# Optimization experiments

Measured on AMD Instinct MI355X. Metric: run time of the kernel, lower is better.

The kernel has to match this reference:

```python
import jax, jax.numpy as jnp
import numpy as np

INPUT_DIM = 6
HIDDEN = 128


def neighbor_mean(x, adj):
    # x: [B,N,F], adj: [B,N,N]; node i averages itself + neighbors (adj>0)
    mask = (adj > 0).astype(x.dtype)  # [B,N,N]
    s = jnp.einsum('bij,bjf->bif', mask, x) + x  # sum neighbors + self
    cnt = mask.sum(-1) + 1.0  # [B,N]
    return s / cnt[..., None]


def lstm_scan(x, Wi, Wh, bi, bh, reverse=False):
    # x: [B,T,F]; Wi: [4H,F]; Wh: [4H,H]; gate order i,f,g,o (torch)
    B, T, F = x.shape
    H = Wh.shape[1]
    xw = jnp.einsum('btf,gf->btg', x, Wi) + bi + bh  # [B,T,4H]
    def step(carry, xt):
        h, c = carry
        z = xt + h @ Wh.T  # [B,4H]
        i, f, g, o = jnp.split(z, 4, axis=-1)
        i = jax.nn.sigmoid(i); f = jax.nn.sigmoid(f)
        g = jnp.tanh(g); o = jax.nn.sigmoid(o)
        c = f * c + i * g
        h = o * jnp.tanh(c)
        return (h, c), h
    init = (jnp.zeros((B, H), x.dtype), jnp.zeros((B, H), x.dtype))
    xs = jnp.swapaxes(xw, 0, 1)  # [T,B,4H]
    (hT, cT), hs = jax.lax.scan(step, init, xs, reverse=reverse)
    return hT


def setup_inputs():
    key = jax.random.key(0)
    ks = jax.random.split(key, 12)
    B, N = 4096, 64
    inp = {
        'device_idx': jax.random.uniform(ks[0], (B,), jnp.float32),
        'matrix': jax.random.uniform(ks[1], (B, N, N), jnp.float32),
        'features': jax.random.normal(ks[2], (B, N, INPUT_DIM), jnp.float32),
    }
    s = 1.0 / np.sqrt(HIDDEN)
    def u(k, shape):
        return jax.random.uniform(k, shape, jnp.float32, -s, s)
    inp['Wi_f'] = u(ks[3], (4 * HIDDEN, INPUT_DIM))
    inp['Wh_f'] = u(ks[4], (4 * HIDDEN, HIDDEN))
    inp['bi_f'] = u(ks[5], (4 * HIDDEN,))
    inp['bh_f'] = u(ks[6], (4 * HIDDEN,))
    inp['Wi_b'] = u(ks[7], (4 * HIDDEN, INPUT_DIM))
    inp['Wh_b'] = u(ks[8], (4 * HIDDEN, HIDDEN))
    inp['bi_b'] = u(ks[9], (4 * HIDDEN,))
    inp['bh_b'] = u(ks[10], (4 * HIDDEN,))
    inp['fc_w'] = u(ks[11], (1, 2 * HIDDEN + 1))
    inp['fc_b'] = jnp.zeros((1,), jnp.float32)
    return inp


def reference(device_idx, matrix, features, Wi_f, Wh_f, bi_f, bh_f, Wi_b, Wh_b, bi_b, bh_b, fc_w, fc_b):
    upd = neighbor_mean(features, matrix)  # [B,N,6]
    h_fwd = lstm_scan(upd, Wi_f, Wh_f, bi_f, bh_f, reverse=False)  # [B,H]
    h_bwd = lstm_scan(upd, Wi_b, Wh_b, bi_b, bh_b, reverse=True)   # [B,H]
    hn = jnp.concatenate([h_fwd, h_bwd], axis=1)  # [B,2H]
    final = jnp.concatenate([device_idx[:, None], hn], axis=1)  # [B,2H+1]
    y = final @ fc_w.T + fc_b
    return y.reshape(-1)
```

## Files before the change

kernel.cpp:

```cpp
#include <hip/hip_runtime.h>
#include <hip/hip_bf16.h>

#define B_TOTAL 4096

typedef short short8 __attribute__((ext_vector_type(8)));
typedef float f32x4 __attribute__((ext_vector_type(4)));
typedef int   i32x4 __attribute__((ext_vector_type(4)));

__device__ __forceinline__ unsigned short rne_bf16(float x) {
    unsigned int u = __float_as_uint(x);
    unsigned int r = (u + 0x7fffu + ((u >> 16) & 1u)) >> 16;
    return (unsigned short)r;
}
__device__ __forceinline__ unsigned int cvt2bf(float lo, float hi) {
    unsigned int r;
    asm("v_cvt_pk_bf16_f32 %0, %1, %2" : "=v"(r) : "v"(lo), "v"(hi));
    return r;
}
__device__ __forceinline__ float fast_sigm(float x) {
    return __builtin_amdgcn_rcpf(1.0f + __expf(-x));
}
__device__ __forceinline__ float fast_tanh(float x) {
    return 1.0f - 2.0f * __builtin_amdgcn_rcpf(1.0f + __expf(2.0f * x));
}
__device__ __forceinline__ void cell_update(const f32x4 z, float& c, float& h) {
    const float ig = fast_sigm(z[0]);
    const float fg = fast_sigm(z[1]);
    const float gg = fast_tanh(z[2]);
    const float og = fast_sigm(z[3]);
    c = fg * c + ig * gg;
    h = og * fast_tanh(c);
}

__global__ __launch_bounds__(256) void k_neighbor_mean(
    const float* __restrict__ matrix,
    const float* __restrict__ features,
    float* __restrict__ upd)
{
    __shared__ float adj[64][65];
    __shared__ float fx[64][6];
    const int b = blockIdx.x;
    const int tid = threadIdx.x;
    const float* mb_ = matrix + (size_t)b * 4096;
    for (int idx = tid; idx < 4096; idx += 256) adj[idx >> 6][idx & 63] = mb_[idx];
    const float* fb = features + (size_t)b * 384;
    for (int idx = tid; idx < 384; idx += 256) fx[idx / 6][idx % 6] = fb[idx];
    __syncthreads();
    if (tid < 64) {
        const int i = tid;
        float s0=0,s1=0,s2=0,s3=0,s4=0,s5=0,cnt=0;
        for (int j = 0; j < 64; j++) {
            float m = adj[i][j] > 0.0f ? 1.0f : 0.0f;
            cnt += m;
            s0 += m*fx[j][0]; s1 += m*fx[j][1]; s2 += m*fx[j][2];
            s3 += m*fx[j][3]; s4 += m*fx[j][4]; s5 += m*fx[j][5];
        }
        const float inv = 1.0f / (cnt + 1.0f);
        float* o = upd + (size_t)b * 384 + i * 6;
        o[0]=(s0+fx[i][0])*inv; o[1]=(s1+fx[i][1])*inv; o[2]=(s2+fx[i][2])*inv;
        o[3]=(s3+fx[i][3])*inv; o[4]=(s4+fx[i][4])*inv; o[5]=(s5+fx[i][5])*inv;
    }
}

__global__ __launch_bounds__(256) void k_wprep4(
    const float* __restrict__ Wi_f, const float* __restrict__ Wh_f,
    const float* __restrict__ bi_f, const float* __restrict__ bh_f,
    const float* __restrict__ Wi_b, const float* __restrict__ Wh_b,
    const float* __restrict__ bi_b, const float* __restrict__ bh_b,
    signed char* __restrict__ Wd1, signed char* __restrict__ Wd2,
    unsigned short* __restrict__ AwU, float* __restrict__ BqO)
{
    const int idx = blockIdx.x * 256 + threadIdx.x;
    if (idx < 131072) {
        const int dir = idx >> 16;
        const int r = idx & 65535;
        const int mtg = r >> 11;
        const int kc  = (r >> 10) & 1;
        const int l   = (r >> 4) & 63;
        const int e   = r & 15;
        const int n = mtg * 16 + (l & 15);
        const int j = ((n & 3) << 7) + (n >> 2);
        const int ks = kc * 64 + 16 * (l >> 4) + e;
        const int hu = 8 * (ks >> 3) + ((ks & 7) >> 1) + 4 * (ks & 1);
        const float w = (dir ? Wh_b : Wh_f)[j * 128 + hu];
        const float a = w * 1024.0f;
        const float r1 = rintf(a);
        Wd1[idx] = (signed char)(int)r1;
        Wd2[idx] = (signed char)(int)rintf((a - r1) * 128.0f);
    } else if (idx < 163840) {
        const int i2 = idx - 131072;
        const int dir = i2 >> 14;
        const int r = i2 & 16383;
        const int mtg = r >> 9, l = (r >> 3) & 63, e = r & 7;
        const int n = mtg * 16 + (l & 15);
        const int j = ((n & 3) << 7) + (n >> 2);
        float w = 0.0f;
        if ((l >> 4) == 0 && e < 6) w = (dir ? Wi_b : Wi_f)[j * 6 + e];
        AwU[i2] = rne_bf16(w);
    } else if (idx < 164864) {
        const int i2 = idx - 163840;
        const int dir = i2 >> 9;
        const int n = i2 & 511;
        const int j = ((n & 3) << 7) + (n >> 2);
        BqO[i2] = (dir ? bi_b : bi_f)[j] + (dir ? bh_b : bh_f)[j];
    }
}

__global__ __launch_bounds__(1024) void k_lstm7(
    const float* __restrict__ upd,
    const signed char* __restrict__ Wd1,
    const signed char* __restrict__ Wd2,
    const unsigned short* __restrict__ AwU,
    const float* __restrict__ Bq,
    float* __restrict__ hout)
{
    __shared__ char Hb[32768];
    __shared__ char Ub[32768];
    const int tid  = threadIdx.x;
    const int wave = tid >> 6;
    const int lane = tid & 63;
    const int dir  = blockIdx.y;
    const int b0   = blockIdx.x * 32;
    const int l15  = lane & 15;
    const int lhi  = lane >> 4;

    i32x4 wd1[2][2], wd2[2][2];
    short8 awu[2];
    f32x4 bias[2];
    #pragma unroll
    for (int mt = 0; mt < 2; mt++) {
        const int mtg = 2 * wave + mt;
        #pragma unroll
        for (int kc = 0; kc < 2; kc++) {
            wd1[mt][kc] = *(const i32x4*)(Wd1 + dir * 65536 + mtg * 2048 + kc * 1024 + lane * 16);
            wd2[mt][kc] = *(const i32x4*)(Wd2 + dir * 65536 + mtg * 2048 + kc * 1024 + lane * 16);
        }
        awu[mt] = *(const short8*)(AwU + dir * 16384 + mtg * 512 + lane * 8);
        bias[mt] = *(const f32x4*)(Bq + dir * 512 + (8 * wave + 4 * mt + lhi) * 4);
    }

    for (int i = tid; i < 2048; i += 1024) {
        const int t = i >> 5, b = i & 31;
        const float2* p = (const float2*)(upd + (size_t)(b0 + b) * 384 + t * 6);
        const float2 a0 = p[0], a1 = p[1], a2 = p[2];
        i32x4 hi4;
        hi4[0] = (int)cvt2bf(a0.x, a0.y);
        hi4[1] = (int)cvt2bf(a1.x, a1.y);
        hi4[2] = (int)cvt2bf(a2.x, a2.y);
        hi4[3] = 0;
        *(i32x4*)(Ub + t * 512 + b * 16) = hi4;
    }
    for (int i = tid; i < 8192; i += 1024) ((int*)Hb)[i] = 0;

    int ra[2], wa[2];
    #pragma unroll
    for (int g = 0; g < 2; g++) {
        ra[g] = g * 16384 + 4096 + l15 * 144 + lhi * 16;
        wa[g] = g * 16384 + l15 * 144 + 8 * wave + 2 * lhi;
    }
    float c00 = 0.0f, c01 = 0.0f, c10 = 0.0f, c11 = 0.0f;
    __syncthreads();

    const i32x4 zi = {0, 0, 0, 0};

    #pragma unroll 1
    for (int s = 0; s < 64; ++s) {
        const int t = dir ? (63 - s) : s;
        const int ub = t * 512;

        const short8 f1g0 = *(const short8*)(Ub + ub + l15 * 16);
        const short8 f1g1 = *(const short8*)(Ub + ub + 256 + l15 * 16);

        __builtin_amdgcn_s_setprio(1);
        i32x4 A[2][2], Bc[2][2];
        f32x4 U[2][2];
        {
            const i32x4 h1k0 = *(const i32x4*)(Hb + ra[0]);
            const i32x4 h1k1 = *(const i32x4*)(Hb + ra[0] + 64);
            const i32x4 h2k0 = *(const i32x4*)(Hb + ra[0] + 8192);
            const i32x4 h2k1 = *(const i32x4*)(Hb + ra[0] + 8256);
            U[0][0] = __builtin_amdgcn_mfma_f32_16x16x32_bf16(awu[0], f1g0, bias[0], 0, 0, 0);
            U[0][1] = __builtin_amdgcn_mfma_f32_16x16x32_bf16(awu[1], f1g0, bias[1], 0, 0, 0);
            #pragma unroll
            for (int mt = 0; mt < 2; mt++) {
                i32x4 a = __builtin_amdgcn_mfma_i32_16x16x64_i8(wd1[mt][0], h1k0, zi, 0, 0, 0);
                a = __builtin_amdgcn_mfma_i32_16x16x64_i8(wd1[mt][1], h1k1, a, 0, 0, 0);
                i32x4 b = __builtin_amdgcn_mfma_i32_16x16x64_i8(wd1[mt][0], h2k0, zi, 0, 0, 0);
                b = __builtin_amdgcn_mfma_i32_16x16x64_i8(wd1[mt][1], h2k1, b, 0, 0, 0);
                b = __builtin_amdgcn_mfma_i32_16x16x64_i8(wd2[mt][0], h1k0, b, 0, 0, 0);
                b = __builtin_amdgcn_mfma_i32_16x16x64_i8(wd2[mt][1], h1k1, b, 0, 0, 0);
                A[0][mt] = a; Bc[0][mt] = b;
            }
        }
        {
            const i32x4 h1k0 = *(const i32x4*)(Hb + ra[1]);
            const i32x4 h1k1 = *(const i32x4*)(Hb + ra[1] + 64);
            const i32x4 h2k0 = *(const i32x4*)(Hb + ra[1] + 8192);
            const i32x4 h2k1 = *(const i32x4*)(Hb + ra[1] + 8256);
            U[1][0] = __builtin_amdgcn_mfma_f32_16x16x32_bf16(awu[0], f1g1, bias[0], 0, 0, 0);
            U[1][1] = __builtin_amdgcn_mfma_f32_16x16x32_bf16(awu[1], f1g1, bias[1], 0, 0, 0);
            #pragma unroll
            for (int mt = 0; mt < 2; mt++) {
                i32x4 a = __builtin_amdgcn_mfma_i32_16x16x64_i8(wd1[mt][0], h1k0, zi, 0, 0, 0);
                a = __builtin_amdgcn_mfma_i32_16x16x64_i8(wd1[mt][1], h1k1, a, 0, 0, 0);
                i32x4 b = __builtin_amdgcn_mfma_i32_16x16x64_i8(wd1[mt][0], h2k0, zi, 0, 0, 0);
                b = __builtin_amdgcn_mfma_i32_16x16x64_i8(wd1[mt][1], h2k1, b, 0, 0, 0);
                b = __builtin_amdgcn_mfma_i32_16x16x64_i8(wd2[mt][0], h1k0, b, 0, 0, 0);
                b = __builtin_amdgcn_mfma_i32_16x16x64_i8(wd2[mt][1], h1k1, b, 0, 0, 0);
                A[1][mt] = a; Bc[1][mt] = b;
            }
        }
        __builtin_amdgcn_s_setprio(0);

        #pragma unroll
        for (int g = 0; g < 2; g++) {
            int d1[2], d2[2];
            float ho[2];
            #pragma unroll
            for (int mt = 0; mt < 2; mt++) {
                f32x4 z;
                #pragma unroll
                for (int i = 0; i < 4; i++)
                    z[i] = U[g][mt][i] + (float)A[g][mt][i] * 0x1p-16f
                                       + (float)Bc[g][mt][i] * 0x1p-23f;
                float& cc = (g == 0) ? (mt == 0 ? c00 : c01) : (mt == 0 ? c10 : c11);
                float h;
                cell_update(z, cc, h);
                ho[mt] = h;
                const float a = h * 64.0f;
                const float r1 = rintf(a);
                d1[mt] = (int)r1;
                d2[mt] = (int)rintf((a - r1) * 128.0f);
            }
            if (s < 63) {
                *(unsigned short*)(Hb + wa[g]) =
                    (unsigned short)((d1[0] & 0xff) | ((d1[1] & 0xff) << 8));
                *(unsigned short*)(Hb + wa[g] + 8192) =
                    (unsigned short)((d2[0] & 0xff) | ((d2[1] & 0xff) << 8));
            } else {
                float* o = hout + ((size_t)dir * B_TOTAL + b0 + g * 16 + l15) * 128;
                o[8 * wave + lhi]     = ho[0];
                o[8 * wave + 4 + lhi] = ho[1];
            }
        }
        ra[0] ^= 0x1000; ra[1] ^= 0x1000;
        wa[0] ^= 0x1000; wa[1] ^= 0x1000;
        __syncthreads();
    }
}

__global__ __launch_bounds__(256) void k_final(
    const float* __restrict__ hout,
    const float* __restrict__ device_idx,
    const float* __restrict__ fc_w,
    const float* __restrict__ fc_b,
    float* __restrict__ y)
{
    const int wave = threadIdx.x >> 6;
    const int lane = threadIdx.x & 63;
    const int b = blockIdx.x * 4 + wave;
    const float* hf = hout + (size_t)b * 128;
    const float* hb = hout + ((size_t)B_TOTAL + b) * 128;
    float p = fc_w[1 + lane]        * hf[lane]
            + fc_w[1 + 64 + lane]   * hf[64 + lane]
            + fc_w[129 + lane]      * hb[lane]
            + fc_w[129 + 64 + lane] * hb[64 + lane];
    #pragma unroll
    for (int off = 32; off; off >>= 1) p += __shfl_xor(p, off, 64);
    if (lane == 0) y[b] = p + fc_w[0] * device_idx[b] + fc_b[0];
}

extern "C" void kernel_launch(void* const* d_in, const int* in_sizes, int n_in,
                              void* d_out, int out_size, void* d_ws, size_t ws_size,
                              hipStream_t stream) {
    const float* device_idx = (const float*)d_in[0];
    const float* matrix     = (const float*)d_in[1];
    const float* features   = (const float*)d_in[2];
    const float* Wi_f = (const float*)d_in[3];
    const float* Wh_f = (const float*)d_in[4];
    const float* bi_f = (const float*)d_in[5];
    const float* bh_f = (const float*)d_in[6];
    const float* Wi_b = (const float*)d_in[7];
    const float* Wh_b = (const float*)d_in[8];
    const float* bi_b = (const float*)d_in[9];
    const float* bh_b = (const float*)d_in[10];
    const float* fc_w = (const float*)d_in[11];
    const float* fc_b = (const float*)d_in[12];
    float* out = (float*)d_out;

    float* ws = (float*)d_ws;
    float*          upd  = ws;
    signed char*    Wd1  = (signed char*)(ws + 1572864);
    signed char*    Wd2  = (signed char*)(ws + 1605632);
    unsigned short* AwU  = (unsigned short*)(ws + 1638400);
    float*          Bq   = ws + 1654784;
    float*          hout = ws + 1655808;

    hipLaunchKernelGGL(k_neighbor_mean, dim3(B_TOTAL), dim3(256), 0, stream,
                       matrix, features, upd);
    hipLaunchKernelGGL(k_wprep4, dim3(644), dim3(256), 0, stream,
                       Wi_f, Wh_f, bi_f, bh_f, Wi_b, Wh_b, bi_b, bh_b,
                       Wd1, Wd2, AwU, Bq);
    hipLaunchKernelGGL(k_lstm7, dim3(B_TOTAL / 32, 2), dim3(1024), 0, stream,
                       upd, Wd1, Wd2, AwU, Bq, hout);
    hipLaunchKernelGGL(k_final, dim3(B_TOTAL / 4), dim3(256), 0, stream,
                       hout, device_idx, fc_w, fc_b, out);
}
```

Measured before the change: 196.7 us.

## Pipeline LSTM batch halves across steps and fold log2e into quantized weights

The LSTM loop now runs over 128 half-steps that alternate between the two 16-batch groups. The MFMA matmuls for the next group are issued while the gate nonlinearities for the current group are computed, so matrix and transcendental work overlap and a barrier is placed after each half-step. The weights and biases are prescaled by log2e (2·log2e for the tanh gate), which lets the gates use exp2 directly. The four gate reciprocals share one rcp through products of the denominators, and hidden-state requantization uses a magic-number float trick. The costs are twice as many barriers, possible precision loss from the product-of-denominators reciprocal and the changed quantization scale, and extra register pressure.

```diff
diff --git a/kernel.cpp b/kernel.cpp
--- a/kernel.cpp
+++ b/kernel.cpp
@@ -2,6 +2,7 @@
 #include <hip/hip_bf16.h>
 
 #define B_TOTAL 4096
+#define LOG2E 1.44269504088896f
 
 typedef short short8 __attribute__((ext_vector_type(8)));
 typedef float f32x4 __attribute__((ext_vector_type(4)));
@@ -16,20 +17,6 @@
     unsigned int r;
     asm("v_cvt_pk_bf16_f32 %0, %1, %2" : "=v"(r) : "v"(lo), "v"(hi));
     return r;
-}
-__device__ __forceinline__ float fast_sigm(float x) {
-    return __builtin_amdgcn_rcpf(1.0f + __expf(-x));
-}
-__device__ __forceinline__ float fast_tanh(float x) {
-    return 1.0f - 2.0f * __builtin_amdgcn_rcpf(1.0f + __expf(2.0f * x));
-}
-__device__ __forceinline__ void cell_update(const f32x4 z, float& c, float& h) {
-    const float ig = fast_sigm(z[0]);
-    const float fg = fast_sigm(z[1]);
-    const float gg = fast_tanh(z[2]);
-    const float og = fast_sigm(z[3]);
-    c = fg * c + ig * gg;
-    h = og * fast_tanh(c);
 }
 
 __global__ __launch_bounds__(256) void k_neighbor_mean(
@@ -62,7 +49,7 @@
     }
 }
 
-__global__ __launch_bounds__(256) void k_wprep4(
+__global__ __launch_bounds__(256) void k_wprep5(
     const float* __restrict__ Wi_f, const float* __restrict__ Wh_f,
     const float* __restrict__ bi_f, const float* __restrict__ bh_f,
     const float* __restrict__ Wi_b, const float* __restrict__ Wh_b,
@@ -81,9 +68,9 @@
         const int n = mtg * 16 + (l & 15);
         const int j = ((n & 3) << 7) + (n >> 2);
         const int ks = kc * 64 + 16 * (l >> 4) + e;
-        const int hu = 8 * (ks >> 3) + ((ks & 7) >> 1) + 4 * (ks & 1);
+        const int hu = 8 * (ks >> 3) + 4 * (ks & 1) + ((ks & 7) >> 1);
         const float w = (dir ? Wh_b : Wh_f)[j * 128 + hu];
-        const float a = w * 1024.0f;
+        const float a = w * (512.0f * LOG2E);
         const float r1 = rintf(a);
         Wd1[idx] = (signed char)(int)r1;
         Wd2[idx] = (signed char)(int)rintf((a - r1) * 128.0f);
@@ -94,19 +81,21 @@
         const int mtg = r >> 9, l = (r >> 3) & 63, e = r & 7;
         const int n = mtg * 16 + (l & 15);
         const int j = ((n & 3) << 7) + (n >> 2);
+        const float sc = ((n & 3) == 2) ? 2.0f * LOG2E : LOG2E;
         float w = 0.0f;
-        if ((l >> 4) == 0 && e < 6) w = (dir ? Wi_b : Wi_f)[j * 6 + e];
+        if ((l >> 4) == 0 && e < 6) w = (dir ? Wi_b : Wi_f)[j * 6 + e] * sc;
         AwU[i2] = rne_bf16(w);
     } else if (idx < 164864) {
         const int i2 = idx - 163840;
         const int dir = i2 >> 9;
         const int n = i2 & 511;
         const int j = ((n & 3) << 7) + (n >> 2);
-        BqO[i2] = (dir ? bi_b : bi_f)[j] + (dir ? bh_b : bh_f)[j];
-    }
-}
-
-__global__ __launch_bounds__(1024) void k_lstm7(
+        const float sc = ((n & 3) == 2) ? 2.0f * LOG2E : LOG2E;
+        BqO[i2] = ((dir ? bi_b : bi_f)[j] + (dir ? bh_b : bh_f)[j]) * sc;
+    }
+}
+
+__global__ __launch_bounds__(1024) void k_lstm8(
     const float* __restrict__ upd,
     const signed char* __restrict__ Wd1,
     const signed char* __restrict__ Wd2,
@@ -114,8 +103,10 @@
     const float* __restrict__ Bq,
     float* __restrict__ hout)
 {
-    __shared__ char Hb[32768];
-    __shared__ char Ub[32768];
+    __shared__ i32x4 HsV[2048];
+    __shared__ i32x4 UsV[2048];
+    char* Hb = (char*)HsV;
+    char* Ub = (char*)UsV;
     const int tid  = threadIdx.x;
     const int wave = tid >> 6;
     const int lane = tid & 63;
@@ -123,6 +114,7 @@
     const int b0   = blockIdx.x * 32;
     const int l15  = lane & 15;
     const int lhi  = lane >> 4;
+    const int hu0  = 8 * wave + lhi, hu1 = hu0 + 4;
 
     i32x4 wd1[2][2], wd2[2][2];
     short8 awu[2];
@@ -135,20 +127,20 @@
             wd1[mt][kc] = *(const i32x4*)(Wd1 + dir * 65536 + mtg * 2048 + kc * 1024 + lane * 16);
             wd2[mt][kc] = *(const i32x4*)(Wd2 + dir * 65536 + mtg * 2048 + kc * 1024 + lane * 16);
         }
-        awu[mt] = *(const short8*)(AwU + dir * 16384 + mtg * 512 + lane * 8);
-        bias[mt] = *(const f32x4*)(Bq + dir * 512 + (8 * wave + 4 * mt + lhi) * 4);
+        awu[mt]  = *(const short8*)(AwU + dir * 16384 + mtg * 512 + lane * 8);
+        bias[mt] = *(const f32x4*)(Bq + dir * 512 + mtg * 16 + 4 * lhi);
     }
 
     for (int i = tid; i < 2048; i += 1024) {
         const int t = i >> 5, b = i & 31;
         const float2* p = (const float2*)(upd + (size_t)(b0 + b) * 384 + t * 6);
         const float2 a0 = p[0], a1 = p[1], a2 = p[2];
-        i32x4 hi4;
-        hi4[0] = (int)cvt2bf(a0.x, a0.y);
-        hi4[1] = (int)cvt2bf(a1.x, a1.y);
-        hi4[2] = (int)cvt2bf(a2.x, a2.y);
-        hi4[3] = 0;
-        *(i32x4*)(Ub + t * 512 + b * 16) = hi4;
+        i32x4 v;
+        v[0] = (int)cvt2bf(a0.x, a0.y);
+        v[1] = (int)cvt2bf(a1.x, a1.y);
+        v[2] = (int)cvt2bf(a2.x, a2.y);
+        v[3] = 0;
+        *(i32x4*)(Ub + (b >> 4) * 16384 + t * 256 + (b & 15) * 16) = v;
     }
     for (int i = tid; i < 8192; i += 1024) ((int*)Hb)[i] = 0;
 
@@ -158,93 +150,115 @@
         ra[g] = g * 16384 + 4096 + l15 * 144 + lhi * 16;
         wa[g] = g * 16384 + l15 * 144 + 8 * wave + 2 * lhi;
     }
-    float c00 = 0.0f, c01 = 0.0f, c10 = 0.0f, c11 = 0.0f;
+    float cs[2][2] = {{0.0f, 0.0f}, {0.0f, 0.0f}};
+    f32x4 Ua[2][2];
+    i32x4 Aa[2][2], Ba[2][2];
     __syncthreads();
 
     const i32x4 zi = {0, 0, 0, 0};
 
-    #pragma unroll 1
-    for (int s = 0; s < 64; ++s) {
-        const int t = dir ? (63 - s) : s;
-        const int ub = t * 512;
-
-        const short8 f1g0 = *(const short8*)(Ub + ub + l15 * 16);
-        const short8 f1g1 = *(const short8*)(Ub + ub + 256 + l15 * 16);
-
-        __builtin_amdgcn_s_setprio(1);
-        i32x4 A[2][2], Bc[2][2];
-        f32x4 U[2][2];
-        {
-            const i32x4 h1k0 = *(const i32x4*)(Hb + ra[0]);
-            const i32x4 h1k1 = *(const i32x4*)(Hb + ra[0] + 64);
-            const i32x4 h2k0 = *(const i32x4*)(Hb + ra[0] + 8192);
-            const i32x4 h2k1 = *(const i32x4*)(Hb + ra[0] + 8256);
-            U[0][0] = __builtin_amdgcn_mfma_f32_16x16x32_bf16(awu[0], f1g0, bias[0], 0, 0, 0);
-            U[0][1] = __builtin_amdgcn_mfma_f32_16x16x32_bf16(awu[1], f1g0, bias[1], 0, 0, 0);
+    {
+        const int tt = dir ? 63 : 0;
+        const short8 fu = *(const short8*)(Ub + tt * 256 + l15 * 16);
+        const i32x4 h1k0 = *(const i32x4*)(Hb + ra[0]);
+        const i32x4 h1k1 = *(const i32x4*)(Hb + ra[0] + 64);
+        const i32x4 h2k0 = *(const i32x4*)(Hb + ra[0] + 8192);
+        const i32x4 h2k1 = *(const i32x4*)(Hb + ra[0] + 8256);
+        ra[0] ^= 0x1000;
+        #pragma unroll
+        for (int mt = 0; mt < 2; mt++) {
+            Ua[0][mt] = __builtin_amdgcn_mfma_f32_16x16x32_bf16(awu[mt], fu, bias[mt], 0, 0, 0);
+            i32x4 a = __builtin_amdgcn_mfma_i32_16x16x64_i8(wd1[mt][0], h1k0, zi, 0, 0, 0);
+            a = __builtin_amdgcn_mfma_i32_16x16x64_i8(wd1[mt][1], h1k1, a, 0, 0, 0);
+            i32x4 b = __builtin_amdgcn_mfma_i32_16x16x64_i8(wd1[mt][0], h2k0, zi, 0, 0, 0);
+            b = __builtin_amdgcn_mfma_i32_16x16x64_i8(wd1[mt][1], h2k1, b, 0, 0, 0);
+            b = __builtin_amdgcn_mfma_i32_16x16x64_i8(wd2[mt][0], h1k0, b, 0, 0, 0);
+            b = __builtin_amdgcn_mfma_i32_16x16x64_i8(wd2[mt][1], h1k1, b, 0, 0, 0);
+            Aa[0][mt] = a; Ba[0][mt] = b;
+        }
+    }
+
+    #pragma unroll 2
+    for (int iv = 0; iv < 128; ++iv) {
+        const int gc = iv & 1;
+        const int sc = iv >> 1;
+
+        float z[2][4];
+        #pragma unroll
+        for (int mt = 0; mt < 2; mt++)
+            #pragma unroll
+            for (int i = 0; i < 4; i++) {
+                const int T = (Aa[gc][mt][i] << 7) + Ba[gc][mt][i];
+                z[mt][i] = fmaf((float)T, (i == 2) ? 0x1p-21f : 0x1p-22f, Ua[gc][mt][i]);
+            }
+
+        if (iv < 127) {
+            const int gi = gc ^ 1;
+            const int si = (iv + 1) >> 1;
+            const int tt = dir ? (63 - si) : si;
+            const short8 fu = *(const short8*)(Ub + gi * 16384 + tt * 256 + l15 * 16);
+            const i32x4 h1k0 = *(const i32x4*)(Hb + ra[gi]);
+            const i32x4 h1k1 = *(const i32x4*)(Hb + ra[gi] + 64);
+            const i32x4 h2k0 = *(const i32x4*)(Hb + ra[gi] + 8192);
+            const i32x4 h2k1 = *(const i32x4*)(Hb + ra[gi] + 8256);
+            ra[gi] ^= 0x1000;
+            __builtin_amdgcn_s_setprio(1);
             #pragma unroll
             for (int mt = 0; mt < 2; mt++) {
+                Ua[gi][mt] = __builtin_amdgcn_mfma_f32_16x16x32_bf16(awu[mt], fu, bias[mt], 0, 0, 0);
                 i32x4 a = __builtin_amdgcn_mfma_i32_16x16x64_i8(wd1[mt][0], h1k0, zi, 0, 0, 0);
                 a = __builtin_amdgcn_mfma_i32_16x16x64_i8(wd1[mt][1], h1k1, a, 0, 0, 0);
                 i32x4 b = __builtin_amdgcn_mfma_i32_16x16x64_i8(wd1[mt][0], h2k0, zi, 0, 0, 0);
                 b = __builtin_amdgcn_mfma_i32_16x16x64_i8(wd1[mt][1], h2k1, b, 0, 0, 0);
                 b = __builtin_amdgcn_mfma_i32_16x16x64_i8(wd2[mt][0], h1k0, b, 0, 0, 0);
                 b = __builtin_amdgcn_mfma_i32_16x16x64_i8(wd2[mt][1], h1k1, b, 0, 0, 0);
-                A[0][mt] = a; Bc[0][mt] = b;
+                Aa[gi][mt] = a; Ba[gi][mt] = b;
             }
-        }
-        {
-            const i32x4 h1k0 = *(const i32x4*)(Hb + ra[1]);
-            const i32x4 h1k1 = *(const i32x4*)(Hb + ra[1] + 64);
-            const i32x4 h2k0 = *(const i32x4*)(Hb + ra[1] + 8192);
-            const i32x4 h2k1 = *(const i32x4*)(Hb + ra[1] + 8256);
-            U[1][0] = __builtin_amdgcn_mfma_f32_16x16x32_bf16(awu[0], f1g1, bias[0], 0, 0, 0);
-            U[1][1] = __builtin_amdgcn_mfma_f32_16x16x32_bf16(awu[1], f1g1, bias[1], 0, 0, 0);
+            __builtin_amdgcn_s_setprio(0);
+        }
+
+        float ig[2], fg[2], gg[2], og[2], Dq[2], hh[2];
+        #pragma unroll
+        for (int mt = 0; mt < 2; mt++) {
+            const float D0 = 1.0f + __builtin_amdgcn_exp2f(-z[mt][0]);
+            const float D1 = 1.0f + __builtin_amdgcn_exp2f(-z[mt][1]);
+            const float D2 = 1.0f + __builtin_amdgcn_exp2f( z[mt][2]);
+            const float D3 = 1.0f + __builtin_amdgcn_exp2f(-z[mt][3]);
+            const float P2 = D0 * D1, P3 = P2 * D2, P4 = P3 * D3;
+            const float r  = __builtin_amdgcn_rcpf(P4);
+            const float Q2 = D3 * D2, Q3 = Q2 * D1;
+            ig[mt] = r * Q3;
+            fg[mt] = (r * Q2) * D0;
+            og[mt] = r * P3;
+            gg[mt] = fmaf(-2.0f, (r * P2) * D3, 1.0f);
+        }
+        #pragma unroll
+        for (int mt = 0; mt < 2; mt++) {
+            cs[gc][mt] = fmaf(fg[mt], cs[gc][mt], ig[mt] * gg[mt]);
+            Dq[mt] = 1.0f + __builtin_amdgcn_exp2f(fminf(cs[gc][mt] * (2.0f * LOG2E), 30.0f));
+        }
+        const float rq = __builtin_amdgcn_rcpf(Dq[0] * Dq[1]);
+        hh[0] = og[0] * fmaf(-2.0f, rq * Dq[1], 1.0f);
+        hh[1] = og[1] * fmaf(-2.0f, rq * Dq[0], 1.0f);
+
+        if (sc < 63) {
+            int d1[2], d2[2];
             #pragma unroll
             for (int mt = 0; mt < 2; mt++) {
-                i32x4 a = __builtin_amdgcn_mfma_i32_16x16x64_i8(wd1[mt][0], h1k0, zi, 0, 0, 0);
-                a = __builtin_amdgcn_mfma_i32_16x16x64_i8(wd1[mt][1], h1k1, a, 0, 0, 0);
-                i32x4 b = __builtin_amdgcn_mfma_i32_16x16x64_i8(wd1[mt][0], h2k0, zi, 0, 0, 0);
-                b = __builtin_amdgcn_mfma_i32_16x16x64_i8(wd1[mt][1], h2k1, b, 0, 0, 0);
-                b = __builtin_amdgcn_mfma_i32_16x16x64_i8(wd2[mt][0], h1k0, b, 0, 0, 0);
-                b = __builtin_amdgcn_mfma_i32_16x16x64_i8(wd2[mt][1], h1k1, b, 0, 0, 0);
-                A[1][mt] = a; Bc[1][mt] = b;
+                const int t = __float_as_int(fmaf(hh[mt], 8192.0f, 12582912.0f)) - 0x4B400000;
+                d1[mt] = (t + 64) >> 7;
+                d2[mt] = t - (d1[mt] << 7);
             }
-        }
-        __builtin_amdgcn_s_setprio(0);
-
-        #pragma unroll
-        for (int g = 0; g < 2; g++) {
-            int d1[2], d2[2];
-            float ho[2];
-            #pragma unroll
-            for (int mt = 0; mt < 2; mt++) {
-                f32x4 z;
-                #pragma unroll
-                for (int i = 0; i < 4; i++)
-                    z[i] = U[g][mt][i] + (float)A[g][mt][i] * 0x1p-16f
-                                       + (float)Bc[g][mt][i] * 0x1p-23f;
-                float& cc = (g == 0) ? (mt == 0 ? c00 : c01) : (mt == 0 ? c10 : c11);
-                float h;
-                cell_update(z, cc, h);
-                ho[mt] = h;
-                const float a = h * 64.0f;
-                const float r1 = rintf(a);
-                d1[mt] = (int)r1;
-                d2[mt] = (int)rintf((a - r1) * 128.0f);
-            }
-            if (s < 63) {
-                *(unsigned short*)(Hb + wa[g]) =
-                    (unsigned short)((d1[0] & 0xff) | ((d1[1] & 0xff) << 8));
-                *(unsigned short*)(Hb + wa[g] + 8192) =
-                    (unsigned short)((d2[0] & 0xff) | ((d2[1] & 0xff) << 8));
-            } else {
-                float* o = hout + ((size_t)dir * B_TOTAL + b0 + g * 16 + l15) * 128;
-                o[8 * wave + lhi]     = ho[0];
-                o[8 * wave + 4 + lhi] = ho[1];
-            }
-        }
-        ra[0] ^= 0x1000; ra[1] ^= 0x1000;
-        wa[0] ^= 0x1000; wa[1] ^= 0x1000;
+            *(unsigned short*)(Hb + wa[gc]) =
+                (unsigned short)__builtin_amdgcn_perm((unsigned)d1[1], (unsigned)d1[0], 0x0400);
+            *(unsigned short*)(Hb + wa[gc] + 8192) =
+                (unsigned short)__builtin_amdgcn_perm((unsigned)d2[1], (unsigned)d2[0], 0x0400);
+        } else {
+            float* o = hout + ((size_t)dir * B_TOTAL + b0 + gc * 16 + l15) * 128;
+            o[hu0] = hh[0];
+            o[hu1] = hh[1];
+        }
+        wa[gc] ^= 0x1000;
         __syncthreads();
     }
 }
@@ -298,10 +312,10 @@
 
     hipLaunchKernelGGL(k_neighbor_mean, dim3(B_TOTAL), dim3(256), 0, stream,
                        matrix, features, upd);
-    hipLaunchKernelGGL(k_wprep4, dim3(644), dim3(256), 0, stream,
+    hipLaunchKernelGGL(k_wprep5, dim3(644), dim3(256), 0, stream,
                        Wi_f, Wh_f, bi_f, bh_f, Wi_b, Wh_b, bi_b, bh_b,
                        Wd1, Wd2, AwU, Bq);
-    hipLaunchKernelGGL(k_lstm7, dim3(B_TOTAL / 32, 2), dim3(1024), 0, stream,
+    hipLaunchKernelGGL(k_lstm8, dim3(B_TOTAL / 32, 2), dim3(1024), 0, stream,
                        upd, Wd1, Wd2, AwU, Bq, hout);
     hipLaunchKernelGGL(k_final, dim3(B_TOTAL / 4), dim3(256), 0, stream,
                        hout, device_idx, fc_w, fc_b, out);
```

New measurement: 163.2 us. 17.1% less time.
